# Kernel tuning notes

Measured on AMD Instinct MI355X. Metric: run time of the kernel, lower is better.

Reference implementation:

```python
import jax, jax.numpy as jnp
import numpy as np

ATTR_LEN = [2, 4, 4, 2, 6]
CUM = np.concatenate(([0], np.cumsum(ATTR_LEN)))  # [0,2,6,10,12,18]
B, S, D, V = 4096, 200, 64, 100000


def setup_inputs() -> dict:
    key = jax.random.key(0)
    ks = jax.random.split(key, 10)
    x = jax.random.randint(ks[0], (B, S), 0, V)
    # one-hot labels per attribute, concatenated -> [B, 18]
    y_parts = []
    for i, al in enumerate(ATTR_LEN):
        lab = jax.random.randint(jax.random.fold_in(ks[1], i), (B,), 0, al)
        y_parts.append(jax.nn.one_hot(lab, al, dtype=jnp.float32))
    y = jnp.concatenate(y_parts, axis=1)
    emb_table = jax.random.normal(ks[2], (V, D), jnp.float32) * 0.02
    emb_table = emb_table.at[0].set(0.0)  # padding_idx=0
    att_w = jax.random.normal(ks[3], (5, D), jnp.float32) * 0.1
    att_b = jax.random.normal(ks[4], (5,), jnp.float32) * 0.1
    W0 = jax.random.normal(ks[5], (ATTR_LEN[0], D), jnp.float32) * 0.1
    W1 = jax.random.normal(ks[6], (ATTR_LEN[1], D), jnp.float32) * 0.1
    W2 = jax.random.normal(ks[7], (ATTR_LEN[2], D), jnp.float32) * 0.1
    W3 = jax.random.normal(ks[8], (ATTR_LEN[3], D), jnp.float32) * 0.1
    W4 = jax.random.normal(ks[9], (ATTR_LEN[4], D), jnp.float32) * 0.1
    return {"x": x, "y": y, "emb_table": emb_table, "att_w": att_w,
            "att_b": att_b, "W0": W0, "W1": W1, "W2": W2, "W3": W3, "W4": W4}


def reference(x, y, emb_table, att_w, att_b, W0, W1, W2, W3, W4):
    embed = emb_table[x]  # [B, S, D] gather (padding row is zero)
    # 5 per-attribute additive tanh-attention heads, batched over k.
    # Softmax over seq axis is independent per head, so stacking is exact.
    att_u = jnp.tanh(jnp.einsum('bsd,kd->bsk', embed, att_w) + att_b)  # [B,S,5]
    score = jax.nn.softmax(att_u, axis=1)                              # [B,S,5]
    user_rep = jnp.einsum('bsd,bsk->bkd', embed, score)                # [B,5,D]
    Ws = [W0, W1, W2, W3, W4]
    # per-task bias-free linear heads, concatenated -> [B, 18]
    W_user = jnp.concatenate([user_rep[:, i] @ Ws[i].T for i in range(5)], axis=1)
    logits = []
    loss = jnp.float32(0.0)
    for i in range(5):
        Wc = W_user[:, CUM[i]:CUM[i + 1]]
        yc = y[:, CUM[i]:CUM[i + 1]]
        # partial_training=False -> ob = ones -> all rows kept;
        # obj = exp(sum(W*y)) / sum_j exp(W_j)  ==  softmax picked at label
        logp = jax.nn.log_softmax(Wc, axis=1)
        loss = loss + (-jnp.sum(logp * yc) / Wc.shape[0])
        logits.append(jax.nn.softmax(Wc, axis=1))
    logit = jnp.concatenate(logits, axis=1)  # [B, 18]
    return logit, loss
```

## Files before the change

### kernel.cpp

```cpp
#include <hip/hip_runtime.h>
#include <math.h>
#include <stdint.h>

#define Bsz 4096
#define Ssz 200
#define Dsz 64
#define NK  5
#define NT  512

typedef _Float16 half_t;
typedef _Float16 h2    __attribute__((ext_vector_type(2)));
typedef _Float16 f16x8 __attribute__((ext_vector_type(8)));
typedef float    f32x4 __attribute__((ext_vector_type(4)));

#define RSTRIDE 72
#define TSTRIDE 232

__device__ inline h2 pk(float a, float b) {
    return __builtin_bit_cast(h2, __builtin_amdgcn_cvt_pkrtz(a, b));
}

__device__ inline float fast_tanh(float x) {
    float e = __expf(-2.0f * fabsf(x));
    float r = (1.0f - e) / (1.0f + e);
    return copysignf(r, x);
}

__global__ void zero_loss_kernel(float* loss) {
    if (threadIdx.x == 0) *loss = 0.0f;
}

__global__ __launch_bounds__(NT, 4) void tan_kernel(
    const int* __restrict__ x, const float* __restrict__ y,
    const float* __restrict__ emb_table,
    const float* __restrict__ att_w, const float* __restrict__ att_b,
    const float* __restrict__ W0, const float* __restrict__ W1,
    const float* __restrict__ W2, const float* __restrict__ W3,
    const float* __restrict__ W4,
    float* __restrict__ out_logit, float* __restrict__ loss_out)
{
    __shared__ alignas(16) half_t embR[208 * RSTRIDE];
    __shared__ alignas(16) half_t embT[64 * TSTRIDE];
    __shared__ alignas(16) float  ovl[1000];
    __shared__ alignas(16) half_t ascore[NK * 240];
    __shared__ alignas(16) half_t awh[NK * RSTRIDE];
    __shared__ alignas(16) int    xs[Ssz];
    __shared__ float wu[18];

    float* att_raw = ovl;

    const int b   = blockIdx.x;
    const int tid = threadIdx.x;
    const int w   = tid >> 6;
    const int l   = tid & 63;
    const int col = l & 15;
    const int kg  = l >> 4;

    if (tid < Ssz) xs[tid] = x[b * Ssz + tid];
    {
        uint4 z = {0u, 0u, 0u, 0u};
        if (tid < 72)
            *(uint4*)((char*)embR + 200 * 144 + tid * 16) = z;
        if (tid >= 72 && tid < 72 + 192) {
            const int idx = tid - 72, row = idx / 3, q = idx - row * 3;
            *(uint4*)((char*)embT + row * 464 + 400 + q * 16) = z;
        }
    }
    if (tid >= 256 && tid < 256 + NK * 32) {
        const int t = tid - 256, row = t >> 5, cp = t & 31;
        h2 v = {(half_t)att_w[row * 64 + 2 * cp],
                (half_t)att_w[row * 64 + 2 * cp + 1]};
        *(h2*)(awh + row * RSTRIDE + 2 * cp) = v;
    }
    __syncthreads();

    {
        float4 v[7];
#pragma unroll
        for (int p = 0; p < 7; ++p) {
            int i = tid + NT * p;
            if (i > Ssz * 16 - 1) i = Ssz * 16 - 1;
            const int s = i >> 4, c = i & 15;
            v[p] = ((const float4*)(emb_table + (size_t)xs[s] * Dsz))[c];
        }
#pragma unroll
        for (int p = 0; p < 7; ++p) {
            const int i = tid + NT * p;
            if (p < 6 || i < Ssz * 16) {
                const int s = i >> 4, c = i & 15;
                h2 lo = pk(v[p].x, v[p].y);
                h2 hi = pk(v[p].z, v[p].w);
                uint2 u = { __builtin_bit_cast(unsigned, lo),
                            __builtin_bit_cast(unsigned, hi) };
                *(uint2*)(embR + s * RSTRIDE + c * 4) = u;
                embT[(4 * c + 0) * TSTRIDE + s] = lo.x;
                embT[(4 * c + 1) * TSTRIDE + s] = lo.y;
                embT[(4 * c + 2) * TSTRIDE + s] = hi.x;
                embT[(4 * c + 3) * TSTRIDE + s] = hi.y;
            }
        }
    }
    __syncthreads();

    {
        const int brow = (col < 5) ? col : 0;
        const f16x8 bw0 = *(const f16x8*)(awh + brow * RSTRIDE + kg * 8);
        const f16x8 bw1 = *(const f16x8*)(awh + brow * RSTRIDE + 32 + kg * 8);
        const float bk = att_b[brow];
        for (int t = w; t < 13; t += 8) {
            const int s = 16 * t + col;
            const f16x8 a0 = *(const f16x8*)(embR + s * RSTRIDE + kg * 8);
            const f16x8 a1 = *(const f16x8*)(embR + s * RSTRIDE + 32 + kg * 8);
            f32x4 acc = {0.f, 0.f, 0.f, 0.f};
            acc = __builtin_amdgcn_mfma_f32_16x16x32_f16(a0, bw0, acc, 0, 0, 0);
            acc = __builtin_amdgcn_mfma_f32_16x16x32_f16(a1, bw1, acc, 0, 0, 0);
            if (col < 5) {
#pragma unroll
                for (int r = 0; r < 4; ++r) {
                    const int srow = 16 * t + 4 * kg + r;
                    if (srow < Ssz)
                        att_raw[col * 200 + srow] = fast_tanh(acc[r] + bk);
                }
            }
        }
    }
    __syncthreads();

    if (w < NK) {
        const int k = w;
        float vals[4];
        float mx = -1e30f;
#pragma unroll
        for (int j = 0; j < 4; ++j) {
            const int s = l + 64 * j;
            vals[j] = (s < Ssz) ? att_raw[k * 200 + s] : -1e30f;
            mx = fmaxf(mx, vals[j]);
        }
#pragma unroll
        for (int m = 32; m >= 1; m >>= 1) mx = fmaxf(mx, __shfl_xor(mx, m));
        float sum = 0.f;
#pragma unroll
        for (int j = 0; j < 4; ++j) {
            vals[j] = __expf(vals[j] - mx);
            sum += vals[j];
        }
#pragma unroll
        for (int m = 32; m >= 1; m >>= 1) sum += __shfl_xor(sum, m);
        const float inv = 1.0f / sum;
#pragma unroll
        for (int j = 0; j < 4; ++j) {
            const int s = l + 64 * j;
            if (s < Ssz)      ascore[k * 240 + s] = (half_t)(vals[j] * inv);
            else if (s < 224) ascore[k * 240 + s] = (half_t)0.0f;
        }
    }
    __syncthreads();

    {
        const int dtile = w & 3, hh = w >> 2;
        const int arow = (col < 5) ? col : 0;
        const int KK0 = hh ? 4 : 0;
        const int NKK = hh ? 3 : 4;
        f32x4 acc = {0.f, 0.f, 0.f, 0.f};
        for (int q = 0; q < NKK; ++q) {
            const int kk = KK0 + q;
            const f16x8 af = *(const f16x8*)(embT + (dtile * 16 + col) * TSTRIDE
                                             + kk * 32 + kg * 8);
            const f16x8 bf = *(const f16x8*)(ascore + arow * 240 + kk * 32 + kg * 8);
            acc = __builtin_amdgcn_mfma_f32_16x16x32_f16(af, bf, acc, 0, 0, 0);
        }
        float* urp = ovl + hh * 320;
        if (col < 5) {
#pragma unroll
            for (int r = 0; r < 4; ++r)
                urp[col * 64 + dtile * 16 + 4 * kg + r] = acc[r];
        }
    }
    __syncthreads();

    if (tid < NK * Dsz) ovl[640 + tid] = ovl[tid] + ovl[320 + tid];
    __syncthreads();

    for (int j = w; j < 18; j += 8) {
        const float* Wp; int gr, c0;
        if      (j < 2)  { gr = 0; c0 = 0;  Wp = W0; }
        else if (j < 6)  { gr = 1; c0 = 2;  Wp = W1; }
        else if (j < 10) { gr = 2; c0 = 6;  Wp = W2; }
        else if (j < 12) { gr = 3; c0 = 10; Wp = W3; }
        else             { gr = 4; c0 = 12; Wp = W4; }
        float p = ovl[640 + gr * 64 + l] * Wp[(j - c0) * Dsz + l];
#pragma unroll
        for (int m = 32; m >= 1; m >>= 1) p += __shfl_xor(p, m);
        if (l == 0) wu[j] = p;
    }
    __syncthreads();

    if (w == 0) {
        float lossb = 0.f;
        if (l < NK) {
            const int LEN[5] = {2, 4, 4, 2, 6};
            const int C0[5]  = {0, 2, 6, 10, 12};
            const int gidx = l, c0 = C0[gidx], len = LEN[gidx];
            float* op = out_logit + (size_t)b * 18;
            const float* yp = y + (size_t)b * 18;
            float mx = -1e30f;
            for (int j = 0; j < len; ++j) mx = fmaxf(mx, wu[c0 + j]);
            float sum = 0.f;
            for (int j = 0; j < len; ++j) sum += __expf(wu[c0 + j] - mx);
            float inv = 1.0f / sum;
            float lse = mx + __logf(sum);
            for (int j = 0; j < len; ++j) {
                op[c0 + j] = __expf(wu[c0 + j] - mx) * inv;
                lossb += (lse - wu[c0 + j]) * yp[c0 + j];
            }
        }
#pragma unroll
        for (int m = 1; m <= 4; m <<= 1) lossb += __shfl_xor(lossb, m);
        if (l == 0) atomicAdd(loss_out, lossb * (1.0f / Bsz));
    }
}

extern "C" void kernel_launch(void* const* d_in, const int* in_sizes, int n_in,
                              void* d_out, int out_size, void* d_ws, size_t ws_size,
                              hipStream_t stream) {
    const int*   x   = (const int*)d_in[0];
    const float* y   = (const float*)d_in[1];
    const float* emb = (const float*)d_in[2];
    const float* aw  = (const float*)d_in[3];
    const float* ab  = (const float*)d_in[4];
    const float* W0  = (const float*)d_in[5];
    const float* W1  = (const float*)d_in[6];
    const float* W2  = (const float*)d_in[7];
    const float* W3  = (const float*)d_in[8];
    const float* W4  = (const float*)d_in[9];
    float* out  = (float*)d_out;
    float* loss = out + (size_t)Bsz * 18;

    zero_loss_kernel<<<1, 64, 0, stream>>>(loss);
    tan_kernel<<<Bsz, NT, 0, stream>>>(x, y, emb, aw, ab,
                                       W0, W1, W2, W3, W4, out, loss);
}
```

Before: 167.7 us.

## Pre-convert embedding table to fp16 and alias row/transposed LDS buffers

Adds a conversion kernel that writes an fp16 copy of the whole embedding table into workspace each call, so the main kernel gathers half as many bytes per row. The row-major and transposed LDS tiles now share one buffer: transposed values are held in registers and written after the attention-score GEMM finishes, which cuts LDS use and lets launch bounds rise to 8 blocks per CU. The cost is a full-table conversion pass (about 25.6MB read and 12.8MB written) on every call, plus more register pressure from holding the transposed fragments.

```diff
diff --git a/kernel.cpp b/kernel.cpp
--- a/kernel.cpp
+++ b/kernel.cpp
@@ -7,15 +7,15 @@
 #define Dsz 64
 #define NK  5
 #define NT  512
+#define RST 72
+#define TST 232
+#define UNIH 14848
 
 typedef _Float16 half_t;
 typedef _Float16 h2    __attribute__((ext_vector_type(2)));
 typedef _Float16 f16x8 __attribute__((ext_vector_type(8)));
 typedef float    f32x4 __attribute__((ext_vector_type(4)));
 
-#define RSTRIDE 72
-#define TSTRIDE 232
-
 __device__ inline h2 pk(float a, float b) {
     return __builtin_bit_cast(h2, __builtin_amdgcn_cvt_pkrtz(a, b));
 }
@@ -30,24 +30,41 @@
     if (threadIdx.x == 0) *loss = 0.0f;
 }
 
-__global__ __launch_bounds__(NT, 4) void tan_kernel(
+__global__ __launch_bounds__(256) void cvt_kernel(const float* __restrict__ src,
+                                                  half_t* __restrict__ dst) {
+    const size_t i = ((size_t)blockIdx.x * 256 + threadIdx.x) * 8;
+    if (i < (size_t)100000 * 64) {
+        float4 v0 = *(const float4*)(src + i);
+        float4 v1 = *(const float4*)(src + i + 4);
+        union { half_t h[8]; uint4 u; } o;
+        o.h[0] = (half_t)v0.x; o.h[1] = (half_t)v0.y;
+        o.h[2] = (half_t)v0.z; o.h[3] = (half_t)v0.w;
+        o.h[4] = (half_t)v1.x; o.h[5] = (half_t)v1.y;
+        o.h[6] = (half_t)v1.z; o.h[7] = (half_t)v1.w;
+        *(uint4*)(dst + i) = o.u;
+    }
+}
+
+template <bool F16TAB>
+__global__ __launch_bounds__(NT, 8) void tan_kernel(
     const int* __restrict__ x, const float* __restrict__ y,
-    const float* __restrict__ emb_table,
+    const float* __restrict__ emb_table, const half_t* __restrict__ tab16,
     const float* __restrict__ att_w, const float* __restrict__ att_b,
     const float* __restrict__ W0, const float* __restrict__ W1,
     const float* __restrict__ W2, const float* __restrict__ W3,
     const float* __restrict__ W4,
     float* __restrict__ out_logit, float* __restrict__ loss_out)
 {
-    __shared__ alignas(16) half_t embR[208 * RSTRIDE];
-    __shared__ alignas(16) half_t embT[64 * TSTRIDE];
+    __shared__ alignas(16) half_t uni[UNIH];
     __shared__ alignas(16) float  ovl[1000];
     __shared__ alignas(16) half_t ascore[NK * 240];
-    __shared__ alignas(16) half_t awh[NK * RSTRIDE];
+    __shared__ alignas(16) half_t awh[NK * RST];
     __shared__ alignas(16) int    xs[Ssz];
     __shared__ float wu[18];
 
-    float* att_raw = ovl;
+    half_t* embR = uni;
+    half_t* embT = uni;
+    float*  att_raw = ovl;
 
     const int b   = blockIdx.x;
     const int tid = threadIdx.x;
@@ -57,24 +74,37 @@
     const int kg  = l >> 4;
 
     if (tid < Ssz) xs[tid] = x[b * Ssz + tid];
-    {
+    if (tid < 192) {
+        const int row = tid / 3, q = tid - row * 3;
         uint4 z = {0u, 0u, 0u, 0u};
-        if (tid < 72)
-            *(uint4*)((char*)embR + 200 * 144 + tid * 16) = z;
-        if (tid >= 72 && tid < 72 + 192) {
-            const int idx = tid - 72, row = idx / 3, q = idx - row * 3;
-            *(uint4*)((char*)embT + row * 464 + 400 + q * 16) = z;
-        }
+        *(uint4*)((char*)embT + row * 464 + 400 + q * 16) = z;
     }
     if (tid >= 256 && tid < 256 + NK * 32) {
         const int t = tid - 256, row = t >> 5, cp = t & 31;
         h2 v = {(half_t)att_w[row * 64 + 2 * cp],
                 (half_t)att_w[row * 64 + 2 * cp + 1]};
-        *(h2*)(awh + row * RSTRIDE + 2 * cp) = v;
-    }
-    __syncthreads();
-
-    {
+        *(h2*)(awh + row * RST + 2 * cp) = v;
+    }
+    __syncthreads();
+
+    if (F16TAB) {
+        uint4 g[4];
+#pragma unroll
+        for (int p = 0; p < 4; ++p) {
+            int i = tid + NT * p;
+            if (i > 1599) i = 1599;
+            const int s = i >> 3, c = i & 7;
+            g[p] = *(const uint4*)(tab16 + (size_t)xs[s] * Dsz + c * 8);
+        }
+#pragma unroll
+        for (int p = 0; p < 4; ++p) {
+            const int i = tid + NT * p;
+            if (p < 3 || i < 1600) {
+                const int s = i >> 3, c = i & 7;
+                *(uint4*)(embR + s * RST + c * 8) = g[p];
+            }
+        }
+    } else {
         float4 v[7];
 #pragma unroll
         for (int p = 0; p < 7; ++p) {
@@ -92,25 +122,33 @@
                 h2 hi = pk(v[p].z, v[p].w);
                 uint2 u = { __builtin_bit_cast(unsigned, lo),
                             __builtin_bit_cast(unsigned, hi) };
-                *(uint2*)(embR + s * RSTRIDE + c * 4) = u;
-                embT[(4 * c + 0) * TSTRIDE + s] = lo.x;
-                embT[(4 * c + 1) * TSTRIDE + s] = lo.y;
-                embT[(4 * c + 2) * TSTRIDE + s] = hi.x;
-                embT[(4 * c + 3) * TSTRIDE + s] = hi.y;
+                *(uint2*)(embR + s * RST + c * 4) = u;
             }
         }
     }
     __syncthreads();
+
+    h2 te[4][4];
+#pragma unroll
+    for (int p = 0; p < 4; ++p) {
+        int t = tid + NT * p;
+        if (t > 1599) t = 1599;
+        const int dp = t & 31, sq = t >> 5;
+#pragma unroll
+        for (int r = 0; r < 4; ++r)
+            te[p][r] = *(const h2*)(embR + (4 * sq + r) * RST + 2 * dp);
+    }
 
     {
         const int brow = (col < 5) ? col : 0;
-        const f16x8 bw0 = *(const f16x8*)(awh + brow * RSTRIDE + kg * 8);
-        const f16x8 bw1 = *(const f16x8*)(awh + brow * RSTRIDE + 32 + kg * 8);
+        const f16x8 bw0 = *(const f16x8*)(awh + brow * RST + kg * 8);
+        const f16x8 bw1 = *(const f16x8*)(awh + brow * RST + 32 + kg * 8);
         const float bk = att_b[brow];
         for (int t = w; t < 13; t += 8) {
-            const int s = 16 * t + col;
-            const f16x8 a0 = *(const f16x8*)(embR + s * RSTRIDE + kg * 8);
-            const f16x8 a1 = *(const f16x8*)(embR + s * RSTRIDE + 32 + kg * 8);
+            const int s  = 16 * t + col;
+            const int sr = (s < Ssz) ? s : (Ssz - 1);
+            const f16x8 a0 = *(const f16x8*)(embR + sr * RST + kg * 8);
+            const f16x8 a1 = *(const f16x8*)(embR + sr * RST + 32 + kg * 8);
             f32x4 acc = {0.f, 0.f, 0.f, 0.f};
             acc = __builtin_amdgcn_mfma_f32_16x16x32_f16(a0, bw0, acc, 0, 0, 0);
             acc = __builtin_amdgcn_mfma_f32_16x16x32_f16(a1, bw1, acc, 0, 0, 0);
@@ -126,6 +164,21 @@
     }
     __syncthreads();
 
+#pragma unroll
+    for (int p = 0; p < 4; ++p) {
+        const int t = tid + NT * p;
+        if (t < 1600) {
+            const int dp = t & 31, sq = t >> 5;
+            h2 lo01 = {te[p][0].x, te[p][1].x}, lo23 = {te[p][2].x, te[p][3].x};
+            h2 hi01 = {te[p][0].y, te[p][1].y}, hi23 = {te[p][2].y, te[p][3].y};
+            uint2 ulo = { __builtin_bit_cast(unsigned, lo01),
+                          __builtin_bit_cast(unsigned, lo23) };
+            uint2 uhi = { __builtin_bit_cast(unsigned, hi01),
+                          __builtin_bit_cast(unsigned, hi23) };
+            *(uint2*)(embT + (2 * dp)     * TST + 4 * sq) = ulo;
+            *(uint2*)(embT + (2 * dp + 1) * TST + 4 * sq) = uhi;
+        }
+    }
     if (w < NK) {
         const int k = w;
         float vals[4];
@@ -164,7 +217,7 @@
         f32x4 acc = {0.f, 0.f, 0.f, 0.f};
         for (int q = 0; q < NKK; ++q) {
             const int kk = KK0 + q;
-            const f16x8 af = *(const f16x8*)(embT + (dtile * 16 + col) * TSTRIDE
+            const f16x8 af = *(const f16x8*)(embT + (dtile * 16 + col) * TST
                                              + kk * 32 + kg * 8);
             const f16x8 bf = *(const f16x8*)(ascore + arow * 240 + kk * 32 + kg * 8);
             acc = __builtin_amdgcn_mfma_f32_16x16x32_f16(af, bf, acc, 0, 0, 0);
@@ -237,6 +290,15 @@
     float* loss = out + (size_t)Bsz * 18;
 
     zero_loss_kernel<<<1, 64, 0, stream>>>(loss);
-    tan_kernel<<<Bsz, NT, 0, stream>>>(x, y, emb, aw, ab,
-                                       W0, W1, W2, W3, W4, out, loss);
-}
+
+    const size_t need = (size_t)100000 * 64 * sizeof(half_t);
+    if (d_ws && ws_size >= need) {
+        half_t* tab16 = (half_t*)d_ws;
+        cvt_kernel<<<(800000 + 255) / 256, 256, 0, stream>>>(emb, tab16);
+        tan_kernel<true><<<Bsz, NT, 0, stream>>>(x, y, emb, tab16, aw, ab,
+                                                 W0, W1, W2, W3, W4, out, loss);
+    } else {
+        tan_kernel<false><<<Bsz, NT, 0, stream>>>(x, y, emb, nullptr, aw, ab,
+                                                  W0, W1, W2, W3, W4, out, loss);
+    }
+}
```

Result: faster. 157.4 us (-6.2%).
